# Optimization experiments

Hardware: AMD Instinct MI355X
Metric: run time of the kernel (lower is better)

Reference implementation:

```python
import jax, jax.numpy as jnp
import numpy as np

N = 2048
C = 1024
B = 4
LN_EPS = 1e-5
SCALE = 1.0 / np.sqrt(N)  # module uses 1/sqrt(n), not 1/sqrt(d)


def setup_inputs() -> dict:
    key = jax.random.key(0)
    ks = jax.random.split(key, 4)
    x = jax.random.normal(ks[0], (B, C, N), dtype=jnp.float32)
    position = jax.random.normal(ks[1], (N, N), dtype=jnp.float32)
    ln_gamma = jnp.ones((C,), dtype=jnp.float32)
    ln_beta = jnp.zeros((C,), dtype=jnp.float32)
    W_qkv = jax.random.normal(ks[2], (3 * C, C), dtype=jnp.float32) / np.sqrt(C)
    b_qkv = jnp.zeros((3 * C,), dtype=jnp.float32)
    return {"x": x, "position": position, "ln_gamma": ln_gamma,
            "ln_beta": ln_beta, "W_qkv": W_qkv, "b_qkv": b_qkv}


def reference(x, position, ln_gamma, ln_beta, W_qkv, b_qkv):
    # x: [B, C, N] -> tokens-last layout; permute to [B, N, C]
    h = jnp.transpose(x, (0, 2, 1))
    # LayerNorm over channel dim
    mu = jnp.mean(h, axis=-1, keepdims=True)
    var = jnp.mean(jnp.square(h - mu), axis=-1, keepdims=True)
    h = (h - mu) * jax.lax.rsqrt(var + LN_EPS) * ln_gamma + ln_beta
    # QKV projection: torch Linear -> h @ W^T + b
    qkv = jnp.einsum('bnc,dc->bnd', h, W_qkv) + b_qkv
    q, k, v = jnp.split(qkv, 3, axis=-1)  # each [B, N, C]
    # scores: [B, N, N] with learned additive position bias
    scores = jnp.einsum('bic,bjc->bij', q, k) * SCALE + position
    attn = jax.nn.softmax(scores, axis=-1)
    out = jnp.einsum('bij,bjc->bic', attn, v)  # [B, N, C]
    return jnp.transpose(out, (0, 2, 1))  # [B, C, N]
```

## Files before the change

### kernel.cpp

```cpp
#include <hip/hip_runtime.h>
#include <stdint.h>

typedef unsigned short u16;
typedef unsigned int u32;

#define NTOK 2048
#define CDIM 1024
#define BSZ  4
#define MTOT (BSZ * NTOK)
#define QKVD 3072
#define SM_SCALE 0.02209708691207961f

typedef __bf16 bf16x8 __attribute__((ext_vector_type(8)));
typedef float f32x4 __attribute__((ext_vector_type(4)));

__device__ __forceinline__ u16 f2bf(float f) {
  u32 u = __float_as_uint(f);
  u += 0x7fffu + ((u >> 16) & 1u);
  return (u16)(u >> 16);
}

__global__ __launch_bounds__(256) void wconv_kernel(const float* __restrict__ W,
                                                    u16* __restrict__ Wb, int n8,
                                                    float* __restrict__ RS) {
  int i = blockIdx.x * 256 + threadIdx.x;
  if (i < MTOT) RS[i] = 0.f;
  if (i >= n8) return;
  const float4* p = (const float4*)W + (size_t)i * 2;
  float4 a = p[0], b = p[1];
  uint4 o;
  o.x = (u32)f2bf(a.x) | ((u32)f2bf(a.y) << 16);
  o.y = (u32)f2bf(a.z) | ((u32)f2bf(a.w) << 16);
  o.z = (u32)f2bf(b.x) | ((u32)f2bf(b.y) << 16);
  o.w = (u32)f2bf(b.z) | ((u32)f2bf(b.w) << 16);
  ((uint4*)Wb)[i] = o;
}

__global__ __launch_bounds__(512) void ln_kernel(const float* __restrict__ x,
                                                 const float* __restrict__ gamma,
                                                 const float* __restrict__ beta,
                                                 u16* __restrict__ h) {
  int blk = blockIdx.x;
  int b = blk >> 6;
  int n0 = (blk & 63) << 5;
  int t = threadIdx.x;
  int nl = t & 31;
  int cp = t >> 5;
  const float* xb = x + (size_t)b * CDIM * NTOK + n0 + nl;

  float v[64];
  float s = 0.f, ss = 0.f;
#pragma unroll
  for (int k = 0; k < 64; ++k) {
    v[k] = xb[(size_t)(cp + (k << 4)) * NTOK];
    s += v[k]; ss += v[k] * v[k];
  }
  __shared__ float ps[16][32], pss[16][32];
  __shared__ float mean_s[32], rstd_s[32];
  ps[cp][nl] = s; pss[cp][nl] = ss;
  __syncthreads();
  if (t < 32) {
    float m = 0.f, q = 0.f;
#pragma unroll
    for (int p = 0; p < 16; ++p) { m += ps[p][t]; q += pss[p][t]; }
    float mu = m * (1.f / CDIM);
    float var = q * (1.f / CDIM) - mu * mu;
    mean_s[t] = mu;
    rstd_s[t] = rsqrtf(var + 1e-5f);
  }
  __syncthreads();
  float mu_n = mean_s[nl], rs_n = rstd_s[nl];

  __shared__ float tile[64][33];
  int tn = t >> 4, cl = t & 15;
#pragma unroll
  for (int kk = 0; kk < 16; ++kk) {
    __syncthreads();
#pragma unroll
    for (int i = 0; i < 4; ++i) {
      int c = (kk << 6) + (i << 4) + cp;
      tile[(i << 4) + cp][nl] = (v[(kk << 2) + i] - mu_n) * rs_n * gamma[c] + beta[c];
    }
    __syncthreads();
    uint2 pk;
    pk.x = (u32)f2bf(tile[(cl << 2) + 0][tn]) | ((u32)f2bf(tile[(cl << 2) + 1][tn]) << 16);
    pk.y = (u32)f2bf(tile[(cl << 2) + 2][tn]) | ((u32)f2bf(tile[(cl << 2) + 3][tn]) << 16);
    *(uint2*)&h[(size_t)(b * NTOK + n0 + tn) * CDIM + (kk << 6) + (cl << 2)] = pk;
  }
}

__device__ __forceinline__ void gld_lds16(const void* g, void* l) {
  __builtin_amdgcn_global_load_lds(
      (const __attribute__((address_space(1))) void*)g,
      (__attribute__((address_space(3))) void*)l, 16, 0, 0);
}

__device__ __forceinline__ void stage128(const char* g, long ld, char* lds, int t) {
  const long rb = (long)(t >> 2) * ld + ((((t & 3) - (t >> 3)) & 3) << 4);
#pragma unroll
  for (int i = 0; i < 2; ++i)
    gld_lds16(g + rb + (long)(i * 64) * ld,
              lds + ((t >> 6) << 10) + (i << 12));
}

template <int EPI>
__global__ __launch_bounds__(256, 3) void gemm_kernel(
    const u16* __restrict__ A, int lda, long sA,
    const u16* __restrict__ B, int ldb, long sB, int K,
    const float* __restrict__ bias,
    const float* __restrict__ pos,
    u16* __restrict__ Cb, int ldc, long sC,
    u16* __restrict__ KD,
    u16* __restrict__ VT,
    float* __restrict__ CT, long sCT,
    float* __restrict__ RS)
{
  __shared__ char smem[32768];

  const int GX = gridDim.x, GY = gridDim.y;
  const int hb = ((int)blockIdx.z * GY + blockIdx.y) * GX + blockIdx.x;
  const int MX = GX >> 3;
  const int k8 = hb & 7, j8 = hb >> 3;
  const int m = k8 * MX + (j8 % MX);
  const int rest = j8 / MX;
  const int n = rest % GY;
  const int bz = rest / GY;

  A += (size_t)bz * sA;
  B += (size_t)bz * sB;
  const int bm0 = m * 128;
  const int bn0 = n * 128;

  const int t = threadIdx.x;
  const int wave = t >> 6;
  const int wm = wave >> 1, wn = wave & 1;
  const int MROW = wm * 64, NCOL = wn * 64;
  const int lr = t & 15, lk = (t & 63) >> 4;
  const int fragoff = lr * 64 + (((lk + (lr >> 1)) & 3) << 4);

  const long lda2 = (long)lda * 2, ldb2 = (long)ldb * 2;
  const char* Agb = (const char*)A + (size_t)bm0 * lda2;
  const char* Bgb = (const char*)B + (size_t)bn0 * ldb2;

  f32x4 acc[4][4];
#pragma unroll
  for (int mm = 0; mm < 4; ++mm)
#pragma unroll
    for (int nn = 0; nn < 4; ++nn) acc[mm][nn] = (f32x4){0.f, 0.f, 0.f, 0.f};

  const int nt = K >> 6;
  for (int kt = 0; kt < nt; ++kt) {
    __syncthreads();
    const long kb = (long)kt * 128;
    stage128(Agb + kb,      lda2, smem,          t);
    stage128(Agb + kb + 64, lda2, smem + 8192,   t);
    stage128(Bgb + kb,      ldb2, smem + 16384,  t);
    stage128(Bgb + kb + 64, ldb2, smem + 24576,  t);
    __syncthreads();

#pragma unroll
    for (int ks = 0; ks < 2; ++ks) {
      const char* Ab = smem + ks * 8192;
      const char* Bb = smem + 16384 + ks * 8192;
      bf16x8 av[4], bv[4];
#pragma unroll
      for (int i = 0; i < 4; ++i)
        av[i] = *(const bf16x8*)(Ab + (MROW + i * 16) * 64 + fragoff);
#pragma unroll
      for (int i = 0; i < 4; ++i)
        bv[i] = *(const bf16x8*)(Bb + (NCOL + i * 16) * 64 + fragoff);
#pragma unroll
      for (int mm = 0; mm < 4; ++mm)
#pragma unroll
        for (int nn = 0; nn < 4; ++nn)
          acc[mm][nn] = __builtin_amdgcn_mfma_f32_16x16x32_bf16(av[mm], bv[nn],
                                                                acc[mm][nn], 0, 0, 0);
    }
  }

#pragma unroll
  for (int mm = 0; mm < 4; ++mm) {
    const int row = bm0 + MROW + mm * 16 + (lk << 2);
    float rs[4] = {0.f, 0.f, 0.f, 0.f};
    float inv[4];
    if (EPI == 2) {
      const float4 rsv = *(const float4*)(RS + (size_t)bz * NTOK + row);
      inv[0] = 1.f / rsv.x; inv[1] = 1.f / rsv.y;
      inv[2] = 1.f / rsv.z; inv[3] = 1.f / rsv.w;
    }
#pragma unroll
    for (int nn = 0; nn < 4; ++nn) {
      const int col = bn0 + NCOL + nn * 16 + lr;
      f32x4 v = acc[mm][nn];
      if (EPI == 0) {
        const float bb = bias[col];
        if (col < CDIM) {
#pragma unroll
          for (int r = 0; r < 4; ++r)
            Cb[(size_t)(row + r) * CDIM + col] = f2bf(v[r] + bb);
        } else if (col < 2 * CDIM) {
          const int c1 = col - CDIM;
#pragma unroll
          for (int r = 0; r < 4; ++r)
            KD[(size_t)(row + r) * CDIM + c1] = f2bf(v[r] + bb);
        } else {
          const int bq = row >> 11;
          const int j = row & (NTOK - 1);
          const int c2 = col - 2 * CDIM;
          uint2 pk;
          pk.x = (u32)f2bf(v[0] + bb) | ((u32)f2bf(v[1] + bb) << 16);
          pk.y = (u32)f2bf(v[2] + bb) | ((u32)f2bf(v[3] + bb) << 16);
          *(uint2*)&VT[((size_t)bq * CDIM + c2) * NTOK + j] = pk;
        }
      } else if (EPI == 1) {
        u16* Cp = Cb + (size_t)bz * sC;
#pragma unroll
        for (int r = 0; r < 4; ++r) {
          float sv = v[r] * SM_SCALE + pos[(size_t)(row + r) * NTOK + col];
          float e = __expf(sv);
          rs[r] += e;
          Cp[(size_t)(row + r) * ldc + col] = f2bf(e);
        }
      } else {
        float* o = CT + (size_t)bz * sCT + (size_t)col * NTOK + row;
        f32x4 w;
        w[0] = v[0] * inv[0]; w[1] = v[1] * inv[1];
        w[2] = v[2] * inv[2]; w[3] = v[3] * inv[3];
        *(f32x4*)o = w;
      }
    }
    if (EPI == 1) {
#pragma unroll
      for (int r = 0; r < 4; ++r) {
#pragma unroll
        for (int mk = 1; mk <= 8; mk <<= 1)
          rs[r] += __shfl_xor(rs[r], mk, 64);
      }
      if (lr == 0) {
        float* rp = RS + (size_t)bz * NTOK + row;
        atomicAdd(rp + 0, rs[0]);
        atomicAdd(rp + 1, rs[1]);
        atomicAdd(rp + 2, rs[2]);
        atomicAdd(rp + 3, rs[3]);
      }
    }
  }
}

extern "C" void kernel_launch(void* const* d_in, const int* in_sizes, int n_in,
                              void* d_out, int out_size, void* d_ws, size_t ws_size,
                              hipStream_t stream) {
  const float* x     = (const float*)d_in[0];
  const float* pos   = (const float*)d_in[1];
  const float* gamma = (const float*)d_in[2];
  const float* beta  = (const float*)d_in[3];
  const float* W     = (const float*)d_in[4];
  const float* bias  = (const float*)d_in[5];
  float* out = (float*)d_out;
  char* ws = (char*)d_ws;

  u16* Wb  = (u16*)(ws);
  u16* h   = (u16*)(ws + (6ll << 20));
  u16* qd  = (u16*)(ws + (22ll << 20));
  u16* kd  = (u16*)(ws + (38ll << 20));
  u16* vT  = (u16*)(ws + (54ll << 20));
  u16* S   = (u16*)(ws + (70ll << 20));
  float* RS = (float*)(ws + (102ll << 20));

  wconv_kernel<<<dim3((QKVD * CDIM / 8 + 255) / 256), 256, 0, stream>>>(
      W, Wb, QKVD * CDIM / 8, RS);
  ln_kernel<<<dim3(BSZ * (NTOK / 32)), 512, 0, stream>>>(x, gamma, beta, h);

  gemm_kernel<0><<<dim3(MTOT / 128, QKVD / 128, 1), 256, 0, stream>>>(
      h, CDIM, 0, Wb, CDIM, 0, CDIM,
      bias, nullptr, qd, CDIM, 0, kd, vT, nullptr, 0, nullptr);

  gemm_kernel<1><<<dim3(NTOK / 128, NTOK / 128, BSZ), 256, 0, stream>>>(
      qd, CDIM, (long)NTOK * CDIM, kd, CDIM, (long)NTOK * CDIM, CDIM,
      nullptr, pos, S, NTOK, (long)NTOK * NTOK, nullptr, nullptr, nullptr, 0, RS);

  gemm_kernel<2><<<dim3(NTOK / 128, CDIM / 128, BSZ), 256, 0, stream>>>(
      S, NTOK, (long)NTOK * NTOK, vT, NTOK, (long)CDIM * NTOK, NTOK,
      nullptr, nullptr, nullptr, 0, 0, nullptr, nullptr, out, (long)CDIM * NTOK, RS);
}
```

Baseline: 172.6 us.

## Use 256x256 8-wave double-buffered pipelined GEMM for QKV and QK^T

Replaces the 128x128 single-buffered GEMM used for the QKV projection and the score computation with a 256x256-tile, 512-thread kernel. It double-buffers 128 KB of LDS with XOR-swizzled layouts and interleaves global-to-LDS prefetch with MFMA phases, using explicit waitcnt, barriers and setprio. The aim is more data reuse per loaded byte and hiding load latency behind compute. The K loop is hard-coded to 16 steps of 64, which matches K=1024 for both uses. The PV GEMM keeps the old kernel under a new name. The large LDS footprint limits occupancy, and the manual sync schedule is fragile.

```diff
diff --git a/kernel.cpp b/kernel.cpp
--- a/kernel.cpp
+++ b/kernel.cpp
@@ -95,27 +95,27 @@
       (__attribute__((address_space(3))) void*)l, 16, 0, 0);
 }
 
-__device__ __forceinline__ void stage128(const char* g, long ld, char* lds, int t) {
-  const long rb = (long)(t >> 2) * ld + ((((t & 3) - (t >> 3)) & 3) << 4);
+__device__ __forceinline__ void stage_half8(const char* g, long ld, char* region,
+                                            int srow0, int scb, int wave) {
 #pragma unroll
   for (int i = 0; i < 2; ++i)
-    gld_lds16(g + rb + (long)(i * 64) * ld,
-              lds + ((t >> 6) << 10) + (i << 12));
+    gld_lds16(g + (long)(srow0 + i * 64) * ld + scb,
+              region + wave * 1024 + i * 8192);
 }
 
 template <int EPI>
-__global__ __launch_bounds__(256, 3) void gemm_kernel(
+__global__ __launch_bounds__(512, 2) void gemm8_kernel(
     const u16* __restrict__ A, int lda, long sA,
-    const u16* __restrict__ B, int ldb, long sB, int K,
+    const u16* __restrict__ B, int ldb, long sB,
     const float* __restrict__ bias,
     const float* __restrict__ pos,
-    u16* __restrict__ Cb, int ldc, long sC,
+    u16* __restrict__ QD,
+    int ldc, long sC,
     u16* __restrict__ KD,
     u16* __restrict__ VT,
-    float* __restrict__ CT, long sCT,
     float* __restrict__ RS)
 {
-  __shared__ char smem[32768];
+  __shared__ char smem[131072];
 
   const int GX = gridDim.x, GY = gridDim.y;
   const int hb = ((int)blockIdx.z * GY + blockIdx.y) * GX + blockIdx.x;
@@ -128,76 +128,110 @@
 
   A += (size_t)bz * sA;
   B += (size_t)bz * sB;
-  const int bm0 = m * 128;
-  const int bn0 = n * 128;
+  const int bm0 = m * 256;
+  const int bn0 = n * 256;
 
   const int t = threadIdx.x;
   const int wave = t >> 6;
-  const int wm = wave >> 1, wn = wave & 1;
-  const int MROW = wm * 64, NCOL = wn * 64;
+  const int wm = wave >> 2;
+  const int wn = wave & 3;
   const int lr = t & 15, lk = (t & 63) >> 4;
-  const int fragoff = lr * 64 + (((lk + (lr >> 1)) & 3) << 4);
+
+  const int xo0 = (lk * 16) ^ ((lr & 7) << 4);
+  const int xo1 = (64 + lk * 16) ^ ((lr & 7) << 4);
+  const int aoff = (wm * 128 + lr) * 128;
+  const int boff = (wn * 64 + lr) * 128;
+
+  const int srow0 = t >> 3;
+  const int scb = (((t & 7) ^ ((t >> 3) & 7)) << 4);
 
   const long lda2 = (long)lda * 2, ldb2 = (long)ldb * 2;
   const char* Agb = (const char*)A + (size_t)bm0 * lda2;
   const char* Bgb = (const char*)B + (size_t)bn0 * ldb2;
 
-  f32x4 acc[4][4];
-#pragma unroll
-  for (int mm = 0; mm < 4; ++mm)
-#pragma unroll
-    for (int nn = 0; nn < 4; ++nn) acc[mm][nn] = (f32x4){0.f, 0.f, 0.f, 0.f};
-
-  const int nt = K >> 6;
-  for (int kt = 0; kt < nt; ++kt) {
-    __syncthreads();
-    const long kb = (long)kt * 128;
-    stage128(Agb + kb,      lda2, smem,          t);
-    stage128(Agb + kb + 64, lda2, smem + 8192,   t);
-    stage128(Bgb + kb,      ldb2, smem + 16384,  t);
-    stage128(Bgb + kb + 64, ldb2, smem + 24576,  t);
-    __syncthreads();
-
-#pragma unroll
-    for (int ks = 0; ks < 2; ++ks) {
-      const char* Ab = smem + ks * 8192;
-      const char* Bb = smem + 16384 + ks * 8192;
-      bf16x8 av[4], bv[4];
-#pragma unroll
-      for (int i = 0; i < 4; ++i)
-        av[i] = *(const bf16x8*)(Ab + (MROW + i * 16) * 64 + fragoff);
-#pragma unroll
-      for (int i = 0; i < 4; ++i)
-        bv[i] = *(const bf16x8*)(Bb + (NCOL + i * 16) * 64 + fragoff);
-#pragma unroll
-      for (int mm = 0; mm < 4; ++mm)
-#pragma unroll
-        for (int nn = 0; nn < 4; ++nn)
-          acc[mm][nn] = __builtin_amdgcn_mfma_f32_16x16x32_bf16(av[mm], bv[nn],
-                                                                acc[mm][nn], 0, 0, 0);
-    }
-  }
-
-#pragma unroll
-  for (int mm = 0; mm < 4; ++mm) {
-    const int row = bm0 + MROW + mm * 16 + (lk << 2);
+#define ST_A(kt, h, buf) stage_half8(Agb + (long)(h) * 128 * lda2 + (long)(kt) * 128, \
+                                     lda2, smem + (buf) * 32768 + (h) * 16384, srow0, scb, wave)
+#define ST_B(kt, h, buf) stage_half8(Bgb + (long)(h) * 128 * ldb2 + (long)(kt) * 128, \
+                                     ldb2, smem + 65536 + (buf) * 32768 + (h) * 16384, srow0, scb, wave)
+
+  f32x4 acc[8][4];
+#pragma unroll
+  for (int mf = 0; mf < 8; ++mf)
+#pragma unroll
+    for (int nf = 0; nf < 4; ++nf) acc[mf][nf] = (f32x4){0.f, 0.f, 0.f, 0.f};
+
+  ST_B(0, 0, 0); ST_B(0, 1, 0); ST_A(0, 0, 0); ST_A(0, 1, 0);
+  ST_B(1, 0, 1); ST_B(1, 1, 1);
+  asm volatile("s_waitcnt vmcnt(4)" ::: "memory");
+  __builtin_amdgcn_sched_barrier(0);
+  __builtin_amdgcn_s_barrier();
+
+  bf16x8 bv[4][2], av[2][2];
+
+#define PH(c, q, RB, STG, VM)                                                    \
+  {                                                                              \
+    if (RB) {                                                                    \
+      _Pragma("unroll") for (int nf = 0; nf < 4; ++nf) {                         \
+        bv[nf][0] = *(const bf16x8*)(smem + 65536 + (c) * 32768 + boff + nf * 2048 + xo0); \
+        bv[nf][1] = *(const bf16x8*)(smem + 65536 + (c) * 32768 + boff + nf * 2048 + xo1); \
+      }                                                                          \
+    }                                                                            \
+    av[0][0] = *(const bf16x8*)(smem + (c) * 32768 + aoff + (2 * (q)) * 2048 + xo0);     \
+    av[0][1] = *(const bf16x8*)(smem + (c) * 32768 + aoff + (2 * (q)) * 2048 + xo1);     \
+    av[1][0] = *(const bf16x8*)(smem + (c) * 32768 + aoff + (2 * (q) + 1) * 2048 + xo0); \
+    av[1][1] = *(const bf16x8*)(smem + (c) * 32768 + aoff + (2 * (q) + 1) * 2048 + xo1); \
+    STG;                                                                         \
+    __builtin_amdgcn_sched_barrier(0);                                           \
+    __builtin_amdgcn_s_barrier();                                                \
+    asm volatile("s_waitcnt lgkmcnt(0)" ::: "memory");                           \
+    __builtin_amdgcn_sched_barrier(0);                                           \
+    __builtin_amdgcn_s_setprio(1);                                               \
+    _Pragma("unroll") for (int i = 0; i < 2; ++i)                                \
+      _Pragma("unroll") for (int nf = 0; nf < 4; ++nf) {                         \
+        acc[2 * (q) + i][nf] = __builtin_amdgcn_mfma_f32_16x16x32_bf16(          \
+            av[i][0], bv[nf][0], acc[2 * (q) + i][nf], 0, 0, 0);                 \
+        acc[2 * (q) + i][nf] = __builtin_amdgcn_mfma_f32_16x16x32_bf16(          \
+            av[i][1], bv[nf][1], acc[2 * (q) + i][nf], 0, 0, 0);                 \
+      }                                                                          \
+    __builtin_amdgcn_s_setprio(0);                                               \
+    VM;                                                                          \
+    __builtin_amdgcn_sched_barrier(0);                                           \
+    __builtin_amdgcn_s_barrier();                                                \
+  }
+
+#pragma unroll 1
+  for (int u = 0; u < 8; ++u) {
+    const bool g = (u < 7);
+    PH(0, 0, 1, { ST_A(2 * u + 1, 0, 1); }, {});
+    PH(0, 1, 0, { ST_A(2 * u + 1, 1, 1); }, {});
+    PH(0, 2, 0, { if (g) ST_B(2 * u + 2, 0, 0); }, {});
+    PH(0, 3, 0, { if (g) ST_B(2 * u + 2, 1, 0); },
+       { if (g) { asm volatile("s_waitcnt vmcnt(4)" ::: "memory"); }
+         else   { asm volatile("s_waitcnt vmcnt(0)" ::: "memory"); } });
+    PH(1, 0, 1, { if (g) ST_A(2 * u + 2, 0, 0); }, {});
+    PH(1, 1, 0, { if (g) ST_A(2 * u + 2, 1, 0); }, {});
+    PH(1, 2, 0, { if (g) ST_B(2 * u + 3, 0, 1); }, {});
+    PH(1, 3, 0, { if (g) ST_B(2 * u + 3, 1, 1); },
+       { if (g) { asm volatile("s_waitcnt vmcnt(4)" ::: "memory"); } });
+  }
+#undef PH
+#undef ST_A
+#undef ST_B
+
+#pragma unroll
+  for (int mf = 0; mf < 8; ++mf) {
+    const int row = bm0 + wm * 128 + mf * 16 + (lk << 2);
     float rs[4] = {0.f, 0.f, 0.f, 0.f};
-    float inv[4];
-    if (EPI == 2) {
-      const float4 rsv = *(const float4*)(RS + (size_t)bz * NTOK + row);
-      inv[0] = 1.f / rsv.x; inv[1] = 1.f / rsv.y;
-      inv[2] = 1.f / rsv.z; inv[3] = 1.f / rsv.w;
-    }
-#pragma unroll
-    for (int nn = 0; nn < 4; ++nn) {
-      const int col = bn0 + NCOL + nn * 16 + lr;
-      f32x4 v = acc[mm][nn];
+#pragma unroll
+    for (int nf = 0; nf < 4; ++nf) {
+      const int col = bn0 + wn * 64 + nf * 16 + lr;
+      f32x4 v = acc[mf][nf];
       if (EPI == 0) {
         const float bb = bias[col];
         if (col < CDIM) {
 #pragma unroll
           for (int r = 0; r < 4; ++r)
-            Cb[(size_t)(row + r) * CDIM + col] = f2bf(v[r] + bb);
+            QD[(size_t)(row + r) * CDIM + col] = f2bf(v[r] + bb);
         } else if (col < 2 * CDIM) {
           const int c1 = col - CDIM;
 #pragma unroll
@@ -212,8 +246,8 @@
           pk.y = (u32)f2bf(v[2] + bb) | ((u32)f2bf(v[3] + bb) << 16);
           *(uint2*)&VT[((size_t)bq * CDIM + c2) * NTOK + j] = pk;
         }
-      } else if (EPI == 1) {
-        u16* Cp = Cb + (size_t)bz * sC;
+      } else {
+        u16* Cp = QD + (size_t)bz * sC;
 #pragma unroll
         for (int r = 0; r < 4; ++r) {
           float sv = v[r] * SM_SCALE + pos[(size_t)(row + r) * NTOK + col];
@@ -221,12 +255,6 @@
           rs[r] += e;
           Cp[(size_t)(row + r) * ldc + col] = f2bf(e);
         }
-      } else {
-        float* o = CT + (size_t)bz * sCT + (size_t)col * NTOK + row;
-        f32x4 w;
-        w[0] = v[0] * inv[0]; w[1] = v[1] * inv[1];
-        w[2] = v[2] * inv[2]; w[3] = v[3] * inv[3];
-        *(f32x4*)o = w;
       }
     }
     if (EPI == 1) {
@@ -247,6 +275,101 @@
   }
 }
 
+__device__ __forceinline__ void stage128(const char* g, long ld, char* lds, int t) {
+  const long rb = (long)(t >> 2) * ld + ((((t & 3) - (t >> 3)) & 3) << 4);
+#pragma unroll
+  for (int i = 0; i < 2; ++i)
+    gld_lds16(g + rb + (long)(i * 64) * ld,
+              lds + ((t >> 6) << 10) + (i << 12));
+}
+
+__global__ __launch_bounds__(256, 3) void gemm_pv_kernel(
+    const u16* __restrict__ A, int lda, long sA,
+    const u16* __restrict__ B, int ldb, long sB, int K,
+    float* __restrict__ CT, long sCT,
+    const float* __restrict__ RS)
+{
+  __shared__ char smem[32768];
+
+  const int GX = gridDim.x, GY = gridDim.y;
+  const int hb = ((int)blockIdx.z * GY + blockIdx.y) * GX + blockIdx.x;
+  const int MX = GX >> 3;
+  const int k8 = hb & 7, j8 = hb >> 3;
+  const int m = k8 * MX + (j8 % MX);
+  const int rest = j8 / MX;
+  const int n = rest % GY;
+  const int bz = rest / GY;
+
+  A += (size_t)bz * sA;
+  B += (size_t)bz * sB;
+  const int bm0 = m * 128;
+  const int bn0 = n * 128;
+
+  const int t = threadIdx.x;
+  const int wave = t >> 6;
+  const int wm = wave >> 1, wn = wave & 1;
+  const int MROW = wm * 64, NCOL = wn * 64;
+  const int lr = t & 15, lk = (t & 63) >> 4;
+  const int fragoff = lr * 64 + (((lk + (lr >> 1)) & 3) << 4);
+
+  const long lda2 = (long)lda * 2, ldb2 = (long)ldb * 2;
+  const char* Agb = (const char*)A + (size_t)bm0 * lda2;
+  const char* Bgb = (const char*)B + (size_t)bn0 * ldb2;
+
+  f32x4 acc[4][4];
+#pragma unroll
+  for (int mm = 0; mm < 4; ++mm)
+#pragma unroll
+    for (int nn = 0; nn < 4; ++nn) acc[mm][nn] = (f32x4){0.f, 0.f, 0.f, 0.f};
+
+  const int nt = K >> 6;
+  for (int kt = 0; kt < nt; ++kt) {
+    __syncthreads();
+    const long kb = (long)kt * 128;
+    stage128(Agb + kb,      lda2, smem,          t);
+    stage128(Agb + kb + 64, lda2, smem + 8192,   t);
+    stage128(Bgb + kb,      ldb2, smem + 16384,  t);
+    stage128(Bgb + kb + 64, ldb2, smem + 24576,  t);
+    __syncthreads();
+
+#pragma unroll
+    for (int ks = 0; ks < 2; ++ks) {
+      const char* Ab = smem + ks * 8192;
+      const char* Bb = smem + 16384 + ks * 8192;
+      bf16x8 av[4], bv[4];
+#pragma unroll
+      for (int i = 0; i < 4; ++i)
+        av[i] = *(const bf16x8*)(Ab + (MROW + i * 16) * 64 + fragoff);
+#pragma unroll
+      for (int i = 0; i < 4; ++i)
+        bv[i] = *(const bf16x8*)(Bb + (NCOL + i * 16) * 64 + fragoff);
+#pragma unroll
+      for (int mm = 0; mm < 4; ++mm)
+#pragma unroll
+        for (int nn = 0; nn < 4; ++nn)
+          acc[mm][nn] = __builtin_amdgcn_mfma_f32_16x16x32_bf16(av[mm], bv[nn],
+                                                                acc[mm][nn], 0, 0, 0);
+    }
+  }
+
+#pragma unroll
+  for (int mm = 0; mm < 4; ++mm) {
+    const int row = bm0 + MROW + mm * 16 + (lk << 2);
+    const float4 rsv = *(const float4*)(RS + (size_t)bz * NTOK + row);
+    float inv[4] = {1.f / rsv.x, 1.f / rsv.y, 1.f / rsv.z, 1.f / rsv.w};
+#pragma unroll
+    for (int nn = 0; nn < 4; ++nn) {
+      const int col = bn0 + NCOL + nn * 16 + lr;
+      f32x4 v = acc[mm][nn];
+      float* o = CT + (size_t)bz * sCT + (size_t)col * NTOK + row;
+      f32x4 w;
+      w[0] = v[0] * inv[0]; w[1] = v[1] * inv[1];
+      w[2] = v[2] * inv[2]; w[3] = v[3] * inv[3];
+      *(f32x4*)o = w;
+    }
+  }
+}
+
 extern "C" void kernel_launch(void* const* d_in, const int* in_sizes, int n_in,
                               void* d_out, int out_size, void* d_ws, size_t ws_size,
                               hipStream_t stream) {
@@ -271,15 +394,15 @@
       W, Wb, QKVD * CDIM / 8, RS);
   ln_kernel<<<dim3(BSZ * (NTOK / 32)), 512, 0, stream>>>(x, gamma, beta, h);
 
-  gemm_kernel<0><<<dim3(MTOT / 128, QKVD / 128, 1), 256, 0, stream>>>(
-      h, CDIM, 0, Wb, CDIM, 0, CDIM,
-      bias, nullptr, qd, CDIM, 0, kd, vT, nullptr, 0, nullptr);
-
-  gemm_kernel<1><<<dim3(NTOK / 128, NTOK / 128, BSZ), 256, 0, stream>>>(
-      qd, CDIM, (long)NTOK * CDIM, kd, CDIM, (long)NTOK * CDIM, CDIM,
-      nullptr, pos, S, NTOK, (long)NTOK * NTOK, nullptr, nullptr, nullptr, 0, RS);
-
-  gemm_kernel<2><<<dim3(NTOK / 128, CDIM / 128, BSZ), 256, 0, stream>>>(
+  gemm8_kernel<0><<<dim3(MTOT / 256, QKVD / 256, 1), 512, 0, stream>>>(
+      h, CDIM, 0, Wb, CDIM, 0,
+      bias, nullptr, qd, 0, 0, kd, vT, nullptr);
+
+  gemm8_kernel<1><<<dim3(NTOK / 256, NTOK / 256, BSZ), 512, 0, stream>>>(
+      qd, CDIM, (long)NTOK * CDIM, kd, CDIM, (long)NTOK * CDIM,
+      nullptr, pos, S, NTOK, (long)NTOK * NTOK, nullptr, nullptr, RS);
+
+  gemm_pv_kernel<<<dim3(NTOK / 128, CDIM / 128, BSZ), 256, 0, stream>>>(
       S, NTOK, (long)NTOK * NTOK, vT, NTOK, (long)CDIM * NTOK, NTOK,
-      nullptr, nullptr, nullptr, 0, 0, nullptr, nullptr, out, (long)CDIM * NTOK, RS);
-}
+      out, (long)CDIM * NTOK, RS);
+}
```

Measured after the change: 179.9 us. 4.2% more time.
